# Kernel optimization log

Hardware: AMD Instinct MI355X
Metric: run time of the kernel (lower is better)

Reference implementation:

```python
import jax, jax.numpy as jnp
import numpy as np

B, S, D, H = 2, 2048, 1024, 16
HD = D // H  # head dim = 64


def setup_inputs() -> dict:
    key = jax.random.key(0)
    ks = jax.random.split(key, 9)
    sc = 1.0 / np.sqrt(D)
    x = jax.random.normal(ks[0], (B, S, D), dtype=jnp.float32)
    # weights stored as (in, out); y = x @ W + b (same math as torch Linear with W.T)
    Wq = jax.random.normal(ks[1], (D, D), dtype=jnp.float32) * sc
    Wk = jax.random.normal(ks[2], (D, D), dtype=jnp.float32) * sc
    Wv = jax.random.normal(ks[3], (D, D), dtype=jnp.float32) * sc
    Wo = jax.random.normal(ks[4], (D, D), dtype=jnp.float32) * sc
    bq = jax.random.normal(ks[5], (D,), dtype=jnp.float32) * 0.01
    bk = jax.random.normal(ks[6], (D,), dtype=jnp.float32) * 0.01
    bv = jax.random.normal(ks[7], (D,), dtype=jnp.float32) * 0.01
    bo = jax.random.normal(ks[8], (D,), dtype=jnp.float32) * 0.01
    return {"x": x, "Wq": Wq, "bq": bq, "Wk": Wk, "bk": bk,
            "Wv": Wv, "bv": bv, "Wo": Wo, "bo": bo}


def reference(x, Wq, bq, Wk, bk, Wv, bv, Wo, bo):
    b, s, d = x.shape
    q = (x @ Wq + bq).reshape(b, s, H, HD)
    k = (x @ Wk + bk).reshape(b, s, H, HD)
    v = (x @ Wv + bv).reshape(b, s, H, HD)
    # [b, h, s, s] scores, scaled by sqrt(head_dim)
    scores = jnp.einsum('bqhd,bkhd->bhqk', q, k) / np.sqrt(HD)
    causal = jnp.triu(jnp.ones((s, s), dtype=bool), k=1)  # True above diagonal
    scores = jnp.where(causal, -jnp.inf, scores)
    w = jax.nn.softmax(scores, axis=-1)  # dropout rate 0 -> identity
    ctx = jnp.einsum('bhqk,bkhd->bqhd', w, v).reshape(b, s, d)
    return ctx @ Wo + bo
```

## Files before the change

### kernel.cpp

```cpp
#include <hip/hip_runtime.h>
#include <math.h>

#define BB 2
#define SS 2048
#define DD 1024
#define HH 16
#define HDIM 64

typedef __bf16 bf16_t;
typedef __attribute__((ext_vector_type(8))) __bf16 bf16x8;
typedef __attribute__((ext_vector_type(4))) __bf16 bf16x4;
typedef __attribute__((ext_vector_type(4))) float f32x4;

__device__ inline bf16_t f2bf(float f) {
    unsigned int x; __builtin_memcpy(&x, &f, 4);
    unsigned int r = (x + 0x7FFFu + ((x >> 16) & 1u)) >> 16;
    unsigned short us = (unsigned short)r;
    bf16_t b; __builtin_memcpy(&b, &us, 2); return b;
}
__device__ inline unsigned int fbits(float f) {
    unsigned int x; __builtin_memcpy(&x, &f, 4); return x;
}
__device__ inline unsigned int pack_bf2(float a, float b) {
    return ((fbits(a) + 0x8000u) >> 16) | ((fbits(b) + 0x8000u) & 0xFFFF0000u);
}
__device__ inline void gload16(const void* g, void* lds_base) {
    __builtin_amdgcn_global_load_lds(
        (const __attribute__((address_space(1))) void*)g,
        (__attribute__((address_space(3))) void*)lds_base, 16, 0, 0);
}

__global__ __launch_bounds__(256)
void prep_kernel(const float* __restrict__ x, bf16_t* __restrict__ xb,
                 const float* __restrict__ W0, const float* __restrict__ W1,
                 const float* __restrict__ W2, const float* __restrict__ W3,
                 bf16x8* __restrict__ P0, bf16x8* __restrict__ P1,
                 bf16x8* __restrict__ P2, bf16x8* __restrict__ P3) {
    const int bid = blockIdx.x, tid = threadIdx.x;
    if (bid < 2048) {
        const int i = bid * 512 + tid;
        #pragma unroll
        for (int u = 0; u < 2; ++u) {
            const int j = i + u * 256;
            const float4 v = reinterpret_cast<const float4*>(x)[j];
            bf16x4 o;
            o.x = f2bf(v.x); o.y = f2bf(v.y); o.z = f2bf(v.z); o.w = f2bf(v.w);
            reinterpret_cast<bf16x4*>(xb)[j] = o;
        }
    } else {
        const int t = (bid - 2048) * 256 + tid;
        const int g = t >> 10, n = t & 1023;
        const float* Ws[4] = {W0, W1, W2, W3};
        bf16x8* Pp[4] = {P0, P1, P2, P3};
        #pragma unroll
        for (int m = 0; m < 4; ++m) {
            bf16x8 v;
            #pragma unroll
            for (int j = 0; j < 8; ++j) v[j] = f2bf(Ws[m][(size_t)(g * 8 + j) * DD + n]);
            Pp[m][(size_t)g * DD + n] = v;
        }
    }
}

__global__ __launch_bounds__(256)
void gemm_qkv(const bf16_t* __restrict__ A,
              const bf16x8* __restrict__ Wp0, const bf16x8* __restrict__ Wp1,
              const bf16x8* __restrict__ Wp2,
              const float* __restrict__ b0, const float* __restrict__ b1,
              const float* __restrict__ b2,
              bf16_t* __restrict__ C0, bf16_t* __restrict__ C1,
              bf16_t* __restrict__ Vt) {
    extern __shared__ char smem[];
    bf16x8 (*As)[8]   = reinterpret_cast<bf16x8(*)[8]>(smem);
    bf16x8 (*Bs)[128] = reinterpret_cast<bf16x8(*)[128]>(smem + 16384);

    const int z = blockIdx.z;
    const bf16x8* Wp = (z == 0) ? Wp0 : (z == 1) ? Wp1 : Wp2;
    const float* bias = (z == 0) ? b0 : (z == 1) ? b1 : b2;

    const int tid = threadIdx.x;
    const int ln = tid & 63, wv = tid >> 6;
    const int quad = ln >> 4, l15 = ln & 15;
    const int wr = wv >> 1, wc = wv & 1;
    const int m0 = blockIdx.y * 128;
    const int n0 = blockIdx.x * 128;

    int arow[4], acl[4], bg[4], bn[4];
    #pragma unroll
    for (int u = 0; u < 4; ++u) {
        const int S = (wv * 4 + u) * 64 + ln;
        arow[u] = S >> 3; acl[u] = (S & 7) ^ (arow[u] & 7);
        bg[u] = S >> 7;   bn[u] = S & 127;
    }

    f32x4 acc[4][4];
    #pragma unroll
    for (int i = 0; i < 4; ++i)
        #pragma unroll
        for (int j = 0; j < 4; ++j) acc[i][j] = (f32x4){0.f, 0.f, 0.f, 0.f};

    for (int k0 = 0; k0 < DD; k0 += 64) {
        __syncthreads();
        const int kg0 = k0 >> 3;
        #pragma unroll
        for (int u = 0; u < 4; ++u) {
            gload16(&A[(size_t)(m0 + arow[u]) * DD + k0 + acl[u] * 8],
                    smem + (size_t)(wv * 4 + u) * 1024);
            gload16(&Wp[(size_t)(kg0 + bg[u]) * DD + n0 + bn[u]],
                    smem + 16384 + (size_t)(wv * 4 + u) * 1024);
        }
        __syncthreads();

        #pragma unroll
        for (int kk = 0; kk < 2; ++kk) {
            bf16x8 fa[4], fb[4];
            #pragma unroll
            for (int mi = 0; mi < 4; ++mi) {
                const int row = wr * 64 + mi * 16 + l15;
                fa[mi] = As[row][(kk * 4 + quad) ^ (row & 7)];
            }
            #pragma unroll
            for (int ni = 0; ni < 4; ++ni)
                fb[ni] = Bs[kk * 4 + quad][wc * 64 + ni * 16 + l15];
            #pragma unroll
            for (int mi = 0; mi < 4; ++mi)
                #pragma unroll
                for (int ni = 0; ni < 4; ++ni)
                    acc[mi][ni] = __builtin_amdgcn_mfma_f32_16x16x32_bf16(
                        fa[mi], fb[ni], acc[mi][ni], 0, 0, 0);
        }
    }

    if (z < 2) {
        bf16_t* C = (z == 0) ? C0 : C1;
        #pragma unroll
        for (int ni = 0; ni < 4; ++ni) {
            const int col = n0 + wc * 64 + ni * 16 + l15;
            const float bv = bias[col];
            #pragma unroll
            for (int mi = 0; mi < 4; ++mi)
                #pragma unroll
                for (int r = 0; r < 4; ++r) {
                    const int row = m0 + wr * 64 + mi * 16 + quad * 4 + r;
                    C[(size_t)row * DD + col] = f2bf(acc[mi][ni][r] + bv);
                }
        }
    } else {
        unsigned short (*T)[136] = reinterpret_cast<unsigned short(*)[136]>(smem);
        __syncthreads();
        #pragma unroll
        for (int ni = 0; ni < 4; ++ni) {
            const int cl = wc * 64 + ni * 16 + l15;
            const float bv = bias[n0 + cl];
            #pragma unroll
            for (int mi = 0; mi < 4; ++mi) {
                const int rl = wr * 64 + mi * 16 + quad * 4;
                uint2 pk;
                pk.x = pack_bf2(acc[mi][ni][0] + bv, acc[mi][ni][1] + bv);
                pk.y = pack_bf2(acc[mi][ni][2] + bv, acc[mi][ni][3] + bv);
                *reinterpret_cast<uint2*>(&T[cl][rl]) = pk;
            }
        }
        __syncthreads();
        const int b = m0 >> 11, s0 = m0 & 2047, h0 = n0 >> 6;
        #pragma unroll
        for (int u = 0; u < 8; ++u) {
            const int c = u * 256 + tid;
            const int s8 = c & 15, nl = c >> 4;
            const bf16x8 v = *reinterpret_cast<const bf16x8*>(&T[nl][s8 * 8]);
            const int bh = b * 16 + h0 + (nl >> 6), d = nl & 63;
            *reinterpret_cast<bf16x8*>(
                &Vt[((size_t)bh * 64 + d) * SS + s0 + s8 * 8]) = v;
        }
    }
}

__global__ __launch_bounds__(256)
void gemm_out(const bf16_t* __restrict__ A, const bf16x8* __restrict__ Wp,
              const float* __restrict__ bias, float* __restrict__ C) {
    __shared__ bf16x8 As[128][8];
    __shared__ bf16x8 Bs[8][64];

    const int tid = threadIdx.x;
    const int ln = tid & 63, wv = tid >> 6;
    const int quad = ln >> 4, l15 = ln & 15;
    const int wr = wv >> 1, wc = wv & 1;
    const int m0 = blockIdx.y * 128;
    const int n0 = blockIdx.x * 64;

    int arow[4], acl[4], bkg[2], bn[2];
    #pragma unroll
    for (int u = 0; u < 4; ++u) {
        const int S = (wv * 4 + u) * 64 + ln;
        arow[u] = S >> 3; acl[u] = (S & 7) ^ (arow[u] & 7);
    }
    #pragma unroll
    for (int u = 0; u < 2; ++u) {
        const int S = (wv * 2 + u) * 64 + ln;
        bkg[u] = S >> 6; bn[u] = S & 63;
    }

    f32x4 acc[4][2];
    #pragma unroll
    for (int i = 0; i < 4; ++i)
        #pragma unroll
        for (int j = 0; j < 2; ++j) acc[i][j] = (f32x4){0.f, 0.f, 0.f, 0.f};

    for (int k0 = 0; k0 < DD; k0 += 64) {
        __syncthreads();
        const int kg0 = k0 >> 3;
        #pragma unroll
        for (int u = 0; u < 4; ++u)
            gload16(&A[(size_t)(m0 + arow[u]) * DD + k0 + acl[u] * 8],
                    (char*)&As[0][0] + (size_t)(wv * 4 + u) * 1024);
        #pragma unroll
        for (int u = 0; u < 2; ++u)
            gload16(&Wp[(size_t)(kg0 + bkg[u]) * DD + n0 + bn[u]],
                    (char*)&Bs[0][0] + (size_t)(wv * 2 + u) * 1024);
        __syncthreads();

        #pragma unroll
        for (int kk = 0; kk < 2; ++kk) {
            bf16x8 fa[4], fb[2];
            #pragma unroll
            for (int mi = 0; mi < 4; ++mi) {
                const int row = wr * 64 + mi * 16 + l15;
                fa[mi] = As[row][(kk * 4 + quad) ^ (row & 7)];
            }
            #pragma unroll
            for (int ni = 0; ni < 2; ++ni)
                fb[ni] = Bs[kk * 4 + quad][wc * 32 + ni * 16 + l15];
            #pragma unroll
            for (int mi = 0; mi < 4; ++mi)
                #pragma unroll
                for (int ni = 0; ni < 2; ++ni)
                    acc[mi][ni] = __builtin_amdgcn_mfma_f32_16x16x32_bf16(
                        fa[mi], fb[ni], acc[mi][ni], 0, 0, 0);
        }
    }

    #pragma unroll
    for (int ni = 0; ni < 2; ++ni) {
        const int col = n0 + wc * 32 + ni * 16 + l15;
        const float bv = bias[col];
        #pragma unroll
        for (int mi = 0; mi < 4; ++mi)
            #pragma unroll
            for (int r = 0; r < 4; ++r) {
                const int row = m0 + wr * 64 + mi * 16 + quad * 4 + r;
                C[(size_t)row * DD + col] = acc[mi][ni][r] + bv;
            }
    }
}

#define SCL 0.18033688f
#define FM  12.0f

__global__ __launch_bounds__(256)
void attn_mfma(const bf16_t* __restrict__ Q, const bf16_t* __restrict__ Kg,
               const bf16_t* __restrict__ Vt, bf16_t* __restrict__ Ctx) {
    __shared__ bf16x8 Ks[128][8];
    __shared__ bf16x8 Vs[128][8];
    __shared__ unsigned short Ps[4][2][16][64];

    const int tid = threadIdx.x;
    const int ln = tid & 63, w = tid >> 6;
    const int quad = ln >> 4, l15 = ln & 15;
    const int bh = blockIdx.x;
    const int tswz = (blockIdx.x + blockIdx.y) & 7;
    const int qt = (blockIdx.y < 8) ? tswz : 15 - tswz;
    const int b = bh >> 4, h = bh & 15;
    const size_t rowbase = (size_t)b * SS;
    const int col0 = h * 64;

    const int krow0 = w * 16 + (ln >> 3);
    const int krow1 = krow0 + 8;
    const int kc0 = (ln & 7) ^ (krow0 & 7);
    const int kc1 = (ln & 7) ^ (krow1 & 7);

    bf16x8 fq[2][2];
    #pragma unroll
    for (int rg = 0; rg < 2; ++rg) {
        const int qrow = qt * 128 + w * 32 + rg * 16 + l15;
        #pragma unroll
        for (int kk = 0; kk < 2; ++kk)
            fq[rg][kk] = *reinterpret_cast<const bf16x8*>(
                &Q[(rowbase + qrow) * DD + col0 + kk * 32 + quad * 8]);
    }

    f32x4 acc_o[2][4];
    #pragma unroll
    for (int rg = 0; rg < 2; ++rg)
        #pragma unroll
        for (int i = 0; i < 4; ++i) acc_o[rg][i] = (f32x4){0.f, 0.f, 0.f, 0.f};
    float lsum[2] = {0.f, 0.f};

    auto stage = [&](int tile, int half) {
        char* kb = (char*)&Ks[half * 64][0] + w * 2048;
        char* vb = (char*)&Vs[half * 64][0] + w * 2048;
        gload16(&Kg[(rowbase + tile * 64 + krow0) * DD + col0 + kc0 * 8], kb);
        gload16(&Kg[(rowbase + tile * 64 + krow1) * DD + col0 + kc1 * 8], kb + 1024);
        gload16(&Vt[((size_t)bh * 64 + krow0) * SS + tile * 64 + kc0 * 8], vb);
        gload16(&Vt[((size_t)bh * 64 + krow1) * SS + tile * 64 + kc1 * 8], vb + 1024);
    };

    const int swz = l15 & 7;

    auto compute_tile = [&](int ro, int dq0, int dq1) {
        const int dq[2] = {dq0, dq1};
        #pragma unroll
        for (int rg = 0; rg < 2; ++rg) {
            if (dq[rg] < 0) continue;
            unsigned short* const psw = &Ps[w][rg][l15][0];
            #pragma unroll
            for (int ni = 0; ni < 4; ++ni) {
                const int slot = ni * 4 + quad;
                unsigned short* pdst = psw + (((slot >> 1) ^ swz) * 8 + (slot & 1) * 4);
                const int g = ni * 16;
                if (g > dq[rg]) {
                    *reinterpret_cast<uint2*>(pdst) = (uint2){0u, 0u};
                    continue;
                }
                f32x4 st = (f32x4){0.f, 0.f, 0.f, 0.f};
                const int krow = ni * 16 + l15;
                #pragma unroll
                for (int kk = 0; kk < 2; ++kk) {
                    const bf16x8 fk = Ks[ro + krow][(kk * 4 + quad) ^ (krow & 7)];
                    st = __builtin_amdgcn_mfma_f32_16x16x32_bf16(fk, fq[rg][kk], st, 0, 0, 0);
                }
                float p[4];
                #pragma unroll
                for (int r = 0; r < 4; ++r) {
                    p[r] = __builtin_amdgcn_exp2f(st[r] * SCL - FM);
                    if (g == dq[rg] && (quad * 4 + r) > l15) p[r] = 0.f;
                }
                lsum[rg] += (p[0] + p[1]) + (p[2] + p[3]);
                uint2 pk;
                pk.x = pack_bf2(p[0], p[1]);
                pk.y = pack_bf2(p[2], p[3]);
                *reinterpret_cast<uint2*>(pdst) = pk;
            }
        }
        #pragma unroll
        for (int kk = 0; kk < 2; ++kk) {
            bf16x8 fp[2];
            #pragma unroll
            for (int rg = 0; rg < 2; ++rg)
                fp[rg] = *reinterpret_cast<const bf16x8*>(
                    &Ps[w][rg][l15][(((kk * 4 + quad) ^ swz) * 8)]);
            #pragma unroll
            for (int nd = 0; nd < 4; ++nd) {
                const int vrow = nd * 16 + l15;
                const bf16x8 fv = Vs[ro + vrow][(kk * 4 + quad) ^ (vrow & 7)];
                if (dq0 >= 0)
                    acc_o[0][nd] = __builtin_amdgcn_mfma_f32_16x16x32_bf16(fv, fp[0], acc_o[0][nd], 0, 0, 0);
                if (dq1 >= 0)
                    acc_o[1][nd] = __builtin_amdgcn_mfma_f32_16x16x32_bf16(fv, fp[1], acc_o[1][nd], 0, 0, 0);
            }
        }
    };

    for (int p = 0; p < qt; ++p) {
        __syncthreads();
        stage(2 * p, 0);
        stage(2 * p + 1, 1);
        __syncthreads();
        compute_tile(0, 112, 112);
        compute_tile(64, 112, 112);
    }
    {
        __syncthreads();
        stage(2 * qt, 0);
        stage(2 * qt + 1, 1);
        __syncthreads();
        const int lq0 = w * 32, lq1 = w * 32 + 16;
        compute_tile(0, lq0, lq1);
        compute_tile(64, lq0 - 64, lq1 - 64);
    }

    #pragma unroll
    for (int rg = 0; rg < 2; ++rg) {
        float s = lsum[rg];
        s += __shfl_xor(s, 16);
        s += __shfl_xor(s, 32);
        const float inv = 1.f / s;
        const size_t orow = (rowbase + qt * 128 + w * 32 + rg * 16 + l15) * DD + col0;
        #pragma unroll
        for (int nd = 0; nd < 4; ++nd) {
            uint2 ov;
            ov.x = pack_bf2(acc_o[rg][nd][0] * inv, acc_o[rg][nd][1] * inv);
            ov.y = pack_bf2(acc_o[rg][nd][2] * inv, acc_o[rg][nd][3] * inv);
            *reinterpret_cast<uint2*>(&Ctx[orow + nd * 16 + quad * 4]) = ov;
        }
    }
}

extern "C" void kernel_launch(void* const* d_in, const int* in_sizes, int n_in,
                              void* d_out, int out_size, void* d_ws, size_t ws_size,
                              hipStream_t stream) {
    const float* x  = (const float*)d_in[0];
    const float* Wq = (const float*)d_in[1];
    const float* bq = (const float*)d_in[2];
    const float* Wk = (const float*)d_in[3];
    const float* bk = (const float*)d_in[4];
    const float* Wv = (const float*)d_in[5];
    const float* bv = (const float*)d_in[6];
    const float* Wo = (const float*)d_in[7];
    const float* bo = (const float*)d_in[8];
    float* out = (float*)d_out;

    const size_t M = (size_t)BB * SS;
    const size_t mat = M * DD;
    const size_t wsz = (size_t)DD * DD;

    bf16_t* ws = (bf16_t*)d_ws;
    bf16_t* xb   = ws;
    bf16_t* Wqp  = ws + mat;
    bf16_t* Wkp  = Wqp + wsz;
    bf16_t* Wvp  = Wkp + wsz;
    bf16_t* Wop  = Wvp + wsz;
    bf16_t* Qb   = Wop + wsz;
    bf16_t* Kb   = Qb + mat;
    bf16_t* Vtb  = Kb + mat;
    bf16_t* Ctxb = Vtb + mat;

    dim3 blk(256);
    hipLaunchKernelGGL(prep_kernel, dim3(2560), blk, 0, stream,
                       x, xb, Wq, Wk, Wv, Wo,
                       (bf16x8*)Wqp, (bf16x8*)Wkp, (bf16x8*)Wvp, (bf16x8*)Wop);

    hipLaunchKernelGGL(gemm_qkv, dim3(DD / 128, M / 128, 3), blk, 34816, stream,
                       xb, (const bf16x8*)Wqp, (const bf16x8*)Wkp, (const bf16x8*)Wvp,
                       bq, bk, bv, Qb, Kb, Vtb);

    hipLaunchKernelGGL(attn_mfma, dim3(BB * HH, SS / 128), blk, 0, stream,
                       Qb, Kb, Vtb, Ctxb);

    hipLaunchKernelGGL(gemm_out, dim3(DD / 64, M / 128), blk, 0, stream,
                       Ctxb, (const bf16x8*)Wop, bo, out);
}
```

Baseline: 198.8 us.

## Double-buffer LDS tiles in QKV GEMM, output GEMM and attention kernels

Adds a second LDS buffer to all three main kernels. The next K-tile (or K/V tile) is issued with async global-to-LDS loads while MFMAs run on the current buffer, so each iteration needs one barrier instead of two. Fragments are read into registers before the prefetch is issued. This is meant to hide global load latency behind compute, at the cost of doubled LDS use (64KB static in gemm_qkv) and more registers, which may lower occupancy.

```diff
diff --git a/kernel.cpp b/kernel.cpp
--- a/kernel.cpp
+++ b/kernel.cpp
@@ -70,9 +70,8 @@
               const float* __restrict__ b2,
               bf16_t* __restrict__ C0, bf16_t* __restrict__ C1,
               bf16_t* __restrict__ Vt) {
-    extern __shared__ char smem[];
-    bf16x8 (*As)[8]   = reinterpret_cast<bf16x8(*)[8]>(smem);
-    bf16x8 (*Bs)[128] = reinterpret_cast<bf16x8(*)[128]>(smem + 16384);
+    __shared__ bf16x8 smem_v[4096];
+    char* const smem = (char*)smem_v;
 
     const int z = blockIdx.z;
     const bf16x8* Wp = (z == 0) ? Wp0 : (z == 1) ? Wp1 : Wp2;
@@ -99,36 +98,46 @@
         #pragma unroll
         for (int j = 0; j < 4; ++j) acc[i][j] = (f32x4){0.f, 0.f, 0.f, 0.f};
 
-    for (int k0 = 0; k0 < DD; k0 += 64) {
-        __syncthreads();
+    auto stage = [&](int k0, int buf) {
+        char* const base = smem + buf * 32768;
         const int kg0 = k0 >> 3;
         #pragma unroll
         for (int u = 0; u < 4; ++u) {
             gload16(&A[(size_t)(m0 + arow[u]) * DD + k0 + acl[u] * 8],
-                    smem + (size_t)(wv * 4 + u) * 1024);
+                    base + (size_t)(wv * 4 + u) * 1024);
             gload16(&Wp[(size_t)(kg0 + bg[u]) * DD + n0 + bn[u]],
-                    smem + 16384 + (size_t)(wv * 4 + u) * 1024);
-        }
-        __syncthreads();
-
+                    base + 16384 + (size_t)(wv * 4 + u) * 1024);
+        }
+    };
+
+    stage(0, 0);
+    __syncthreads();
+    int cur = 0;
+    for (int t = 0; t < 16; ++t) {
+        const bf16x8 (*As)[8]   = reinterpret_cast<const bf16x8(*)[8]>(smem + cur * 32768);
+        const bf16x8 (*Bs)[128] = reinterpret_cast<const bf16x8(*)[128]>(smem + cur * 32768 + 16384);
+        bf16x8 fa[2][4], fb[2][4];
         #pragma unroll
         for (int kk = 0; kk < 2; ++kk) {
-            bf16x8 fa[4], fb[4];
             #pragma unroll
             for (int mi = 0; mi < 4; ++mi) {
                 const int row = wr * 64 + mi * 16 + l15;
-                fa[mi] = As[row][(kk * 4 + quad) ^ (row & 7)];
+                fa[kk][mi] = As[row][(kk * 4 + quad) ^ (row & 7)];
             }
             #pragma unroll
             for (int ni = 0; ni < 4; ++ni)
-                fb[ni] = Bs[kk * 4 + quad][wc * 64 + ni * 16 + l15];
+                fb[kk][ni] = Bs[kk * 4 + quad][wc * 64 + ni * 16 + l15];
+        }
+        if (t < 15) stage((t + 1) * 64, cur ^ 1);
+        #pragma unroll
+        for (int kk = 0; kk < 2; ++kk)
             #pragma unroll
             for (int mi = 0; mi < 4; ++mi)
                 #pragma unroll
                 for (int ni = 0; ni < 4; ++ni)
                     acc[mi][ni] = __builtin_amdgcn_mfma_f32_16x16x32_bf16(
-                        fa[mi], fb[ni], acc[mi][ni], 0, 0, 0);
-        }
+                        fa[kk][mi], fb[kk][ni], acc[mi][ni], 0, 0, 0);
+        if (t < 15) { __syncthreads(); cur ^= 1; }
     }
 
     if (z < 2) {
@@ -178,8 +187,8 @@
 __global__ __launch_bounds__(256)
 void gemm_out(const bf16_t* __restrict__ A, const bf16x8* __restrict__ Wp,
               const float* __restrict__ bias, float* __restrict__ C) {
-    __shared__ bf16x8 As[128][8];
-    __shared__ bf16x8 Bs[8][64];
+    __shared__ bf16x8 As[2][128][8];
+    __shared__ bf16x8 Bs[2][8][64];
 
     const int tid = threadIdx.x;
     const int ln = tid & 63, wv = tid >> 6;
@@ -206,37 +215,44 @@
         #pragma unroll
         for (int j = 0; j < 2; ++j) acc[i][j] = (f32x4){0.f, 0.f, 0.f, 0.f};
 
-    for (int k0 = 0; k0 < DD; k0 += 64) {
-        __syncthreads();
+    auto stage = [&](int k0, int buf) {
         const int kg0 = k0 >> 3;
         #pragma unroll
         for (int u = 0; u < 4; ++u)
             gload16(&A[(size_t)(m0 + arow[u]) * DD + k0 + acl[u] * 8],
-                    (char*)&As[0][0] + (size_t)(wv * 4 + u) * 1024);
+                    (char*)&As[buf][0][0] + (size_t)(wv * 4 + u) * 1024);
         #pragma unroll
         for (int u = 0; u < 2; ++u)
             gload16(&Wp[(size_t)(kg0 + bkg[u]) * DD + n0 + bn[u]],
-                    (char*)&Bs[0][0] + (size_t)(wv * 2 + u) * 1024);
-        __syncthreads();
-
+                    (char*)&Bs[buf][0][0] + (size_t)(wv * 2 + u) * 1024);
+    };
+
+    stage(0, 0);
+    __syncthreads();
+    int cur = 0;
+    for (int t = 0; t < 16; ++t) {
+        bf16x8 fa[2][4], fb[2][2];
         #pragma unroll
         for (int kk = 0; kk < 2; ++kk) {
-            bf16x8 fa[4], fb[2];
             #pragma unroll
             for (int mi = 0; mi < 4; ++mi) {
                 const int row = wr * 64 + mi * 16 + l15;
-                fa[mi] = As[row][(kk * 4 + quad) ^ (row & 7)];
+                fa[kk][mi] = As[cur][row][(kk * 4 + quad) ^ (row & 7)];
             }
             #pragma unroll
             for (int ni = 0; ni < 2; ++ni)
-                fb[ni] = Bs[kk * 4 + quad][wc * 32 + ni * 16 + l15];
+                fb[kk][ni] = Bs[cur][kk * 4 + quad][wc * 32 + ni * 16 + l15];
+        }
+        if (t < 15) stage((t + 1) * 64, cur ^ 1);
+        #pragma unroll
+        for (int kk = 0; kk < 2; ++kk)
             #pragma unroll
             for (int mi = 0; mi < 4; ++mi)
                 #pragma unroll
                 for (int ni = 0; ni < 2; ++ni)
                     acc[mi][ni] = __builtin_amdgcn_mfma_f32_16x16x32_bf16(
-                        fa[mi], fb[ni], acc[mi][ni], 0, 0, 0);
-        }
+                        fa[kk][mi], fb[kk][ni], acc[mi][ni], 0, 0, 0);
+        if (t < 15) { __syncthreads(); cur ^= 1; }
     }
 
     #pragma unroll
@@ -259,8 +275,8 @@
 __global__ __launch_bounds__(256)
 void attn_mfma(const bf16_t* __restrict__ Q, const bf16_t* __restrict__ Kg,
                const bf16_t* __restrict__ Vt, bf16_t* __restrict__ Ctx) {
-    __shared__ bf16x8 Ks[128][8];
-    __shared__ bf16x8 Vs[128][8];
+    __shared__ bf16x8 Ks[2][128][8];
+    __shared__ bf16x8 Vs[2][128][8];
     __shared__ unsigned short Ps[4][2][16][64];
 
     const int tid = threadIdx.x;
@@ -295,9 +311,9 @@
         for (int i = 0; i < 4; ++i) acc_o[rg][i] = (f32x4){0.f, 0.f, 0.f, 0.f};
     float lsum[2] = {0.f, 0.f};
 
-    auto stage = [&](int tile, int half) {
-        char* kb = (char*)&Ks[half * 64][0] + w * 2048;
-        char* vb = (char*)&Vs[half * 64][0] + w * 2048;
+    auto stage = [&](int tile, int half, int buf) {
+        char* kb = (char*)&Ks[buf][half * 64][0] + w * 2048;
+        char* vb = (char*)&Vs[buf][half * 64][0] + w * 2048;
         gload16(&Kg[(rowbase + tile * 64 + krow0) * DD + col0 + kc0 * 8], kb);
         gload16(&Kg[(rowbase + tile * 64 + krow1) * DD + col0 + kc1 * 8], kb + 1024);
         gload16(&Vt[((size_t)bh * 64 + krow0) * SS + tile * 64 + kc0 * 8], vb);
@@ -306,7 +322,7 @@
 
     const int swz = l15 & 7;
 
-    auto compute_tile = [&](int ro, int dq0, int dq1) {
+    auto compute_tile = [&](int buf, int ro, int dq0, int dq1) {
         const int dq[2] = {dq0, dq1};
         #pragma unroll
         for (int rg = 0; rg < 2; ++rg) {
@@ -325,7 +341,7 @@
                 const int krow = ni * 16 + l15;
                 #pragma unroll
                 for (int kk = 0; kk < 2; ++kk) {
-                    const bf16x8 fk = Ks[ro + krow][(kk * 4 + quad) ^ (krow & 7)];
+                    const bf16x8 fk = Ks[buf][ro + krow][(kk * 4 + quad) ^ (krow & 7)];
                     st = __builtin_amdgcn_mfma_f32_16x16x32_bf16(fk, fq[rg][kk], st, 0, 0, 0);
                 }
                 float p[4];
@@ -351,7 +367,7 @@
             #pragma unroll
             for (int nd = 0; nd < 4; ++nd) {
                 const int vrow = nd * 16 + l15;
-                const bf16x8 fv = Vs[ro + vrow][(kk * 4 + quad) ^ (vrow & 7)];
+                const bf16x8 fv = Vs[buf][ro + vrow][(kk * 4 + quad) ^ (vrow & 7)];
                 if (dq0 >= 0)
                     acc_o[0][nd] = __builtin_amdgcn_mfma_f32_16x16x32_bf16(fv, fp[0], acc_o[0][nd], 0, 0, 0);
                 if (dq1 >= 0)
@@ -360,22 +376,22 @@
         }
     };
 
+    stage(0, 0, 0);
+    stage(1, 1, 0);
+    __syncthreads();
+    int cur = 0;
     for (int p = 0; p < qt; ++p) {
+        stage(2 * (p + 1), 0, cur ^ 1);
+        stage(2 * (p + 1) + 1, 1, cur ^ 1);
+        compute_tile(cur, 0, 112, 112);
+        compute_tile(cur, 64, 112, 112);
         __syncthreads();
-        stage(2 * p, 0);
-        stage(2 * p + 1, 1);
-        __syncthreads();
-        compute_tile(0, 112, 112);
-        compute_tile(64, 112, 112);
+        cur ^= 1;
     }
     {
-        __syncthreads();
-        stage(2 * qt, 0);
-        stage(2 * qt + 1, 1);
-        __syncthreads();
         const int lq0 = w * 32, lq1 = w * 32 + 16;
-        compute_tile(0, lq0, lq1);
-        compute_tile(64, lq0 - 64, lq1 - 64);
+        compute_tile(cur, 0, lq0, lq1);
+        compute_tile(cur, 64, lq0 - 64, lq1 - 64);
     }
 
     #pragma unroll
@@ -429,7 +445,7 @@
                        x, xb, Wq, Wk, Wv, Wo,
                        (bf16x8*)Wqp, (bf16x8*)Wkp, (bf16x8*)Wvp, (bf16x8*)Wop);
 
-    hipLaunchKernelGGL(gemm_qkv, dim3(DD / 128, M / 128, 3), blk, 34816, stream,
+    hipLaunchKernelGGL(gemm_qkv, dim3(DD / 128, M / 128, 3), blk, 0, stream,
                        xb, (const bf16x8*)Wqp, (const bf16x8*)Wkp, (const bf16x8*)Wvp,
                        bq, bk, bv, Qb, Kb, Vtb);
 
```

Result: faster. 188.8 us (-5.1%).
